# Kernel tuning notes

Hardware: AMD Instinct MI355X
Metric: run time of the kernel (lower is better)

Reference implementation:

```python
import jax, jax.numpy as jnp
import numpy as np

N_HEADS = 16
N_KV_HEADS = 4
HEAD_DIM = 128
ROPE_BASE = 10000.0


def _rms_norm(x):
    eps = jnp.asarray(jnp.finfo(x.dtype).eps, x.dtype)
    return x * jax.lax.rsqrt(jnp.mean(x * x, axis=-1, keepdims=True) + eps)


def _rope_tables(T, dtype):
    d = HEAD_DIM
    inv_freq = 1.0 / (ROPE_BASE ** (jnp.arange(0, d, 2, dtype=jnp.float32) / d))
    freqs = jnp.outer(jnp.arange(T, dtype=jnp.float32), inv_freq)  # [T, d/2]
    return jnp.cos(freqs).astype(dtype), jnp.sin(freqs).astype(dtype)


def _apply_rope(x, cos, sin):
    # x: [B, H, T, D]; cos/sin: [T, D/2]
    d = x.shape[-1] // 2
    x1, x2 = x[..., :d], x[..., d:]
    return jnp.concatenate((x1 * cos + x2 * sin, -x1 * sin + x2 * cos), axis=-1)


def setup_inputs() -> dict:
    key = jax.random.key(0)
    ks = jax.random.split(key, 5)
    B, T, C = 2, 2048, 2048
    kv_dim = N_KV_HEADS * HEAD_DIM
    s = 0.02
    return {
        "x": jax.random.normal(ks[0], (B, T, C), jnp.float32),
        "Wq": jax.random.normal(ks[1], (C, C), jnp.float32) * s,
        "Wk": jax.random.normal(ks[2], (kv_dim, C), jnp.float32) * s,
        "Wv": jax.random.normal(ks[3], (kv_dim, C), jnp.float32) * s,
        "Wo": jax.random.normal(ks[4], (C, C), jnp.float32) * s,
    }


def reference(x, Wq, Wk, Wv, Wo):
    B, T, C = x.shape
    g = N_HEADS // N_KV_HEADS

    # QKV projections (torch Linear: x @ W.T), split into heads -> [B, H, T, D]
    q = (x @ Wq.T).reshape(B, T, N_HEADS, HEAD_DIM).transpose(0, 2, 1, 3)
    k = (x @ Wk.T).reshape(B, T, N_KV_HEADS, HEAD_DIM).transpose(0, 2, 1, 3)
    v = (x @ Wv.T).reshape(B, T, N_KV_HEADS, HEAD_DIM).transpose(0, 2, 1, 3)

    # QK RMSNorm (no learned weight)
    q, k = _rms_norm(q), _rms_norm(k)

    # RoPE
    cos, sin = _rope_tables(T, q.dtype)
    q, k = _apply_rope(q, cos, sin), _apply_rope(k, cos, sin)

    # GQA: expand kv heads
    k = jnp.repeat(k, g, axis=1)
    v = jnp.repeat(v, g, axis=1)

    # causal SDPA
    scale = 1.0 / jnp.sqrt(jnp.asarray(HEAD_DIM, q.dtype))
    scores = jnp.einsum("bhqd,bhkd->bhqk", q, k) * scale
    mask = jnp.tril(jnp.ones((T, T), bool))
    scores = jnp.where(mask, scores, jnp.asarray(-jnp.inf, scores.dtype))
    att = jax.nn.softmax(scores, axis=-1)
    y = jnp.einsum("bhqk,bhkd->bhqd", att, v)

    y = y.transpose(0, 2, 1, 3).reshape(B, T, C)
    return y @ Wo.T
```

## Files before the change

### kernel.cpp

```cpp
#include <hip/hip_runtime.h>
#include <hip/hip_bf16.h>
#include <cstdint>
#include <math.h>

#define DEVINL __device__ __forceinline__

typedef __attribute__((ext_vector_type(8))) __bf16 bf16x8;
typedef __attribute__((ext_vector_type(4))) float floatx4;

constexpr int TB = 2;
constexpr int TT = 2048;
constexpr int TC = 2048;
constexpr int NH = 16, NKV = 4, HD = 128;
constexpr int MR = TB * TT;
constexpr int NQ = NH * HD;
constexpr int NK = NKV * HD;
constexpr int NQKV = NQ + 2 * NK;

DEVINL unsigned bfbits(float f) {
  unsigned u = __builtin_bit_cast(unsigned, f);
  return (u + 0x7FFFu + ((u >> 16) & 1u)) >> 16;
}
DEVINL int pack2bf(float lo, float hi) {
  return (int)(bfbits(lo) | (bfbits(hi) << 16));
}
DEVINL void gl_lds16(const __hip_bfloat16* g, __hip_bfloat16* l) {
  __builtin_amdgcn_global_load_lds(
      (const __attribute__((address_space(1))) unsigned int*)g,
      (__attribute__((address_space(3))) unsigned int*)l, 16, 0, 0);
}
DEVINL floatx4 mfma16(bf16x8 a, bf16x8 b, floatx4 c) {
  return __builtin_amdgcn_mfma_f32_16x16x32_bf16(a, b, c, 0, 0, 0);
}
DEVINL void cstore(float* p, float v) { *p = v; }
DEVINL void cstore(__hip_bfloat16* p, float v) { *(unsigned short*)p = (unsigned short)bfbits(v); }

__global__ __launch_bounds__(256) void k_cvt5(
    const float* __restrict__ s0, const float* __restrict__ s1,
    const float* __restrict__ s2, const float* __restrict__ s3,
    const float* __restrict__ s4,
    __hip_bfloat16* __restrict__ d0, __hip_bfloat16* __restrict__ d1,
    __hip_bfloat16* __restrict__ d2, __hip_bfloat16* __restrict__ d3,
    __hip_bfloat16* __restrict__ d4) {
  const float* s;
  __hip_bfloat16* d;
  int n;
  switch (blockIdx.y) {
    case 0: s = s0; d = d0; n = MR * TC; break;
    case 1: s = s1; d = d1; n = NQ * TC; break;
    case 2: s = s2; d = d2; n = NK * TC; break;
    case 3: s = s3; d = d3; n = NK * TC; break;
    default: s = s4; d = d4; n = TC * TC; break;
  }
  int i = (blockIdx.x * 256 + threadIdx.x) * 4;
  if (i >= n) return;
  float4 v = *(const float4*)(s + i);
  ushort4 o;
  o.x = (unsigned short)bfbits(v.x);
  o.y = (unsigned short)bfbits(v.y);
  o.z = (unsigned short)bfbits(v.z);
  o.w = (unsigned short)bfbits(v.w);
  *(ushort4*)(d + i) = o;
}

template <typename OUT_T>
__global__ __launch_bounds__(256, 2) void k_gemm_bt(
    const __hip_bfloat16* __restrict__ A, const __hip_bfloat16* __restrict__ B,
    OUT_T* __restrict__ C, int M, int N, int K) {
  __shared__ __align__(16) __hip_bfloat16 As[128 * 32];
  __shared__ __align__(16) __hip_bfloat16 Bs[128 * 32];
  const int tid = threadIdx.x;
  const int lane = tid & 63, w = tid >> 6;
  const int q15 = lane & 15, quad = lane >> 4;
  const int wm = w >> 1, wn = w & 1;
  const int tm = blockIdx.y, tn = blockIdx.x;

  const int r0 = tid >> 2, c0 = (tid & 3) * 8;
  const __hip_bfloat16* a0 = A + (size_t)(tm * 128 + r0) * K + c0;
  const __hip_bfloat16* a1 = A + (size_t)(tm * 128 + r0 + 64) * K + c0;
  const __hip_bfloat16* b0 = B + (size_t)(tn * 128 + r0) * K + c0;
  const __hip_bfloat16* b1 = B + (size_t)(tn * 128 + r0 + 64) * K + c0;
  __hip_bfloat16* lA0 = As + (tid & ~63) * 8;
  __hip_bfloat16* lA1 = As + 2048 + (tid & ~63) * 8;
  __hip_bfloat16* lB0 = Bs + (tid & ~63) * 8;
  __hip_bfloat16* lB1 = Bs + 2048 + (tid & ~63) * 8;

  floatx4 acc[4][4] = {};
  for (int k0 = 0; k0 < K; k0 += 32) {
    __syncthreads();
    gl_lds16(a0 + k0, lA0);
    gl_lds16(a1 + k0, lA1);
    gl_lds16(b0 + k0, lB0);
    gl_lds16(b1 + k0, lB1);
    __syncthreads();
    bf16x8 af[4], bfr[4];
#pragma unroll
    for (int i = 0; i < 4; i++)
      af[i] = *(const bf16x8*)(As + (wm * 64 + i * 16 + q15) * 32 + quad * 8);
#pragma unroll
    for (int i = 0; i < 4; i++)
      bfr[i] = *(const bf16x8*)(Bs + (wn * 64 + i * 16 + q15) * 32 + quad * 8);
#pragma unroll
    for (int mi = 0; mi < 4; mi++)
#pragma unroll
      for (int ni = 0; ni < 4; ni++)
        acc[mi][ni] = mfma16(af[mi], bfr[ni], acc[mi][ni]);
  }
#pragma unroll
  for (int mi = 0; mi < 4; mi++) {
    int row0 = tm * 128 + wm * 64 + mi * 16 + quad * 4;
#pragma unroll
    for (int ni = 0; ni < 4; ni++) {
      int col = tn * 128 + wn * 64 + ni * 16 + q15;
#pragma unroll
      for (int r = 0; r < 4; r++)
        cstore(C + (size_t)(row0 + r) * N + col, acc[mi][ni][r]);
    }
  }
}

__global__ __launch_bounds__(256) void k_ropenorm(
    const __hip_bfloat16* __restrict__ qkv,
    __hip_bfloat16* __restrict__ q_l, __hip_bfloat16* __restrict__ k_l) {
  int gw = (blockIdx.x * 256 + threadIdx.x) >> 6;
  int lane = threadIdx.x & 63;
  int head = gw % 20;
  int bt = gw / 20;
  int b = bt >> 11, t = bt & (TT - 1);
  bool isq = head < NH;
  int h = isq ? head : head - NH;
  const __hip_bfloat16* src = qkv + (size_t)bt * NQKV + (isq ? h * HD : NQ + h * HD);
  float x1 = __bfloat162float(src[lane]);
  float x2 = __bfloat162float(src[lane + 64]);
  float ss = x1 * x1 + x2 * x2;
#pragma unroll
  for (int m = 1; m < 64; m <<= 1) ss += __shfl_xor(ss, m, 64);
  float rinv = rsqrtf(ss * (1.0f / 128.0f) + 1.1920928955078125e-07f);
  float ang = (float)t * exp2f((float)lane * -(13.287712379549449f / 64.0f));
  float sv = sinf(ang), cv = cosf(ang);
  float scale = isq ? (1.4426950408889634f * 0.08838834764831845f) : 1.0f;
  float o1 = (x1 * cv + x2 * sv) * rinv * scale;
  float o2 = (x2 * cv - x1 * sv) * rinv * scale;
  __hip_bfloat16* dst = isq ? q_l + ((size_t)(b * NH + h) * TT + t) * HD
                            : k_l + ((size_t)(b * NKV + h) * TT + t) * HD;
  *(unsigned short*)(dst + lane) = (unsigned short)bfbits(o1);
  *(unsigned short*)(dst + lane + 64) = (unsigned short)bfbits(o2);
}

__global__ __launch_bounds__(256) void k_vtrans(const __hip_bfloat16* __restrict__ qkv,
                                                __hip_bfloat16* __restrict__ vt) {
  __shared__ __hip_bfloat16 tile[64][130];
  int bid = blockIdx.x;
  int t0 = (bid & 31) * 64;
  int hk = (bid >> 5) & 3;
  int b = bid >> 7;
  int tid = threadIdx.x;
#pragma unroll
  for (int j = 0; j < 32; j++) {
    int e = j * 256 + tid;
    int tt = e >> 7, d = e & 127;
    tile[tt][d] = qkv[(size_t)(b * TT + t0 + tt) * NQKV + NQ + NK + hk * HD + d];
  }
  __syncthreads();
#pragma unroll
  for (int j = 0; j < 32; j++) {
    int e = j * 256 + tid;
    int d = e >> 6, tt = e & 63;
    vt[(((size_t)(b * NKV + hk)) * HD + d) * TT + t0 + tt] = tile[tt][d];
  }
}

__global__ __launch_bounds__(256, 2) void k_attn(
    const __hip_bfloat16* __restrict__ q_l, const __hip_bfloat16* __restrict__ k_l,
    const __hip_bfloat16* __restrict__ vt_l, __hip_bfloat16* __restrict__ y) {
  __shared__ __align__(16) __hip_bfloat16 Ks[2][64 * 128];
  __shared__ __align__(16) __hip_bfloat16 Vs[2][128 * 64];
  const int tid = threadIdx.x, lane = tid & 63, w = tid >> 6;
  const int q15 = lane & 15, quad = lane >> 4;
  const int p = blockIdx.x;
  const int h = blockIdx.y, b = blockIdx.z;
  const int hk = h >> 2;

  const __hip_bfloat16* kbase = k_l + (size_t)(b * NKV + hk) * TT * HD;
  const __hip_bfloat16* vbase = vt_l + (size_t)(b * NKV + hk) * HD * TT;

  auto stage = [&](int kb, int buf) {
#pragma unroll
    for (int i = 0; i < 4; i++) {
      int s = i * 256 + tid;
      int rk = s >> 4, ck = s & 15;
      gl_lds16(kbase + (size_t)(kb * 64 + rk) * HD + (ck ^ (rk & 15)) * 8,
               Ks[buf] + (i * 256 + (tid & ~63)) * 8);
      int rv = s >> 3, cv = s & 7;
      gl_lds16(vbase + (size_t)rv * TT + kb * 64 + (cv ^ (rv & 7)) * 8,
               Vs[buf] + (i * 256 + (tid & ~63)) * 8);
    }
  };

  const int s0lane = ((quad & 1) << 1) * 16 + q15;
  const int s1lane = s0lane + 16;
  const bool hi = quad >= 2;
  int cur = 0;

  for (int ph = 0; ph < 2; ph++) {
    const int qb = ph ? (TT / 64 - 1 - p) : p;
    const __hip_bfloat16* qbase = q_l + ((size_t)(b * NH + h) * TT + qb * 64) * HD;

    bf16x8 qf[4];
#pragma unroll
    for (int dc = 0; dc < 4; dc++)
      qf[dc] = *(const bf16x8*)(qbase + (size_t)(w * 16 + q15) * HD + dc * 32 + quad * 8);

    floatx4 ot[8] = {};
    float m_run = -INFINITY, l_run = 0.0f;

    for (int kb = 0; kb <= qb; kb++) {
      __syncthreads();
      if (kb == 0) {
        stage(0, cur);
        __syncthreads();
      }
      if (kb < qb) stage(kb + 1, cur ^ 1);

      floatx4 st[4] = {};
#pragma unroll
      for (int kt = 0; kt < 4; kt++) {
        int r = kt * 16 + q15;
#pragma unroll
        for (int dc = 0; dc < 4; dc++) {
          int c = dc * 4 + quad;
          bf16x8 kf = *(const bf16x8*)(Ks[cur] + (r * 16 + (c ^ (r & 15))) * 8);
          st[kt] = mfma16(kf, qf[dc], st[kt]);
        }
      }
      if (kb == qb) {
        int qg = w * 16 + q15;
#pragma unroll
        for (int kt = 0; kt < 4; kt++)
#pragma unroll
          for (int r = 0; r < 4; r++)
            if (kt * 16 + quad * 4 + r > qg) st[kt][r] = -INFINITY;
      }
      float mloc = -INFINITY;
#pragma unroll
      for (int kt = 0; kt < 4; kt++)
#pragma unroll
        for (int r = 0; r < 4; r++) mloc = fmaxf(mloc, st[kt][r]);
      mloc = fmaxf(mloc, __shfl_xor(mloc, 16, 64));
      mloc = fmaxf(mloc, __shfl_xor(mloc, 32, 64));
      float m_new = fmaxf(m_run, mloc);
      float rsum = 0.f;
      int pk[4][2];
#pragma unroll
      for (int kt = 0; kt < 4; kt++) {
        float p0 = exp2f(st[kt][0] - m_new);
        float p1 = exp2f(st[kt][1] - m_new);
        float p2 = exp2f(st[kt][2] - m_new);
        float p3 = exp2f(st[kt][3] - m_new);
        rsum += (p0 + p1) + (p2 + p3);
        pk[kt][0] = pack2bf(p0, p1);
        pk[kt][1] = pack2bf(p2, p3);
      }
      rsum += __shfl_xor(rsum, 16, 64);
      rsum += __shfl_xor(rsum, 32, 64);
      if (__any(m_new > m_run)) {
        float alpha = exp2f(m_run - m_new);
        l_run *= alpha;
#pragma unroll
        for (int dt = 0; dt < 8; dt++) {
          ot[dt][0] *= alpha; ot[dt][1] *= alpha;
          ot[dt][2] *= alpha; ot[dt][3] *= alpha;
        }
      }
      l_run += rsum;
      m_run = m_new;

#pragma unroll
      for (int kc = 0; kc < 2; kc++) {
        int lo0 = __shfl(pk[kc * 2][0], s0lane, 64);
        int lo1 = __shfl(pk[kc * 2][1], s0lane, 64);
        int lo2 = __shfl(pk[kc * 2][0], s1lane, 64);
        int lo3 = __shfl(pk[kc * 2][1], s1lane, 64);
        int h0 = __shfl(pk[kc * 2 + 1][0], s0lane, 64);
        int h1 = __shfl(pk[kc * 2 + 1][1], s0lane, 64);
        int h2 = __shfl(pk[kc * 2 + 1][0], s1lane, 64);
        int h3 = __shfl(pk[kc * 2 + 1][1], s1lane, 64);
        union { int i[4]; bf16x8 v; } pu;
        pu.i[0] = hi ? h0 : lo0;
        pu.i[1] = hi ? h1 : lo1;
        pu.i[2] = hi ? h2 : lo2;
        pu.i[3] = hi ? h3 : lo3;
        bf16x8 pf = pu.v;
#pragma unroll
        for (int dt = 0; dt < 8; dt++) {
          int r = dt * 16 + q15, c = kc * 4 + quad;
          bf16x8 vf = *(const bf16x8*)(Vs[cur] + (r * 8 + (c ^ (r & 7))) * 8);
          ot[dt] = mfma16(vf, pf, ot[dt]);
        }
      }
      cur ^= 1;
    }
    float linv = 1.0f / l_run;
    int t = qb * 64 + w * 16 + q15;
    __hip_bfloat16* yrow = y + (size_t)(b * TT + t) * TC + h * HD;
#pragma unroll
    for (int dt = 0; dt < 8; dt++) {
      int d = dt * 16 + quad * 4;
      ushort4 o;
      o.x = (unsigned short)bfbits(ot[dt][0] * linv);
      o.y = (unsigned short)bfbits(ot[dt][1] * linv);
      o.z = (unsigned short)bfbits(ot[dt][2] * linv);
      o.w = (unsigned short)bfbits(ot[dt][3] * linv);
      *(ushort4*)(yrow + d) = o;
    }
  }
}

extern "C" void kernel_launch(void* const* d_in, const int* in_sizes, int n_in,
                              void* d_out, int out_size, void* d_ws, size_t ws_size,
                              hipStream_t stream) {
  (void)in_sizes; (void)n_in; (void)out_size; (void)ws_size;
  const float* x  = (const float*)d_in[0];
  const float* Wq = (const float*)d_in[1];
  const float* Wk = (const float*)d_in[2];
  const float* Wv = (const float*)d_in[3];
  const float* Wo = (const float*)d_in[4];
  float* out = (float*)d_out;

  char* ws = (char*)d_ws;
  size_t off = 0;
  auto alloc = [&](size_t bytes) {
    void* p = ws + off;
    off += (bytes + 255) & ~(size_t)255;
    return p;
  };
  __hip_bfloat16* xb   = (__hip_bfloat16*)alloc((size_t)MR * TC * 2);
  __hip_bfloat16* wqkv = (__hip_bfloat16*)alloc((size_t)NQKV * TC * 2);
  __hip_bfloat16* wo   = (__hip_bfloat16*)alloc((size_t)TC * TC * 2);
  __hip_bfloat16* qkv  = (__hip_bfloat16*)alloc((size_t)MR * NQKV * 2);
  __hip_bfloat16* q_l  = (__hip_bfloat16*)alloc((size_t)TB * NH * TT * HD * 2);
  __hip_bfloat16* k_l  = (__hip_bfloat16*)alloc((size_t)TB * NKV * TT * HD * 2);
  __hip_bfloat16* vt_l = (__hip_bfloat16*)alloc((size_t)TB * NKV * HD * TT * 2);
  __hip_bfloat16* yb   = (__hip_bfloat16*)alloc((size_t)MR * TC * 2);

  k_cvt5<<<dim3((MR * TC / 4 + 255) / 256, 5), 256, 0, stream>>>(
      x, Wq, Wk, Wv, Wo,
      xb, wqkv, wqkv + (size_t)NQ * TC, wqkv + (size_t)(NQ + NK) * TC, wo);

  k_gemm_bt<__hip_bfloat16><<<dim3(NQKV / 128, MR / 128), 256, 0, stream>>>(
      xb, wqkv, qkv, MR, NQKV, TC);

  k_ropenorm<<<(MR * 20) / 4, 256, 0, stream>>>(qkv, q_l, k_l);
  k_vtrans<<<TB * NKV * (TT / 64), 256, 0, stream>>>(qkv, vt_l);

  k_attn<<<dim3(TT / 64 / 2, NH, TB), 256, 0, stream>>>(q_l, k_l, vt_l, yb);

  k_gemm_bt<float><<<dim3(TC / 128, MR / 128), 256, 0, stream>>>(
      yb, wo, out, MR, TC, TC);
}
```

Baseline: 330.9 us.

## Drop online-softmax max tracking using bounded normalized scores; fuse prep kernels

Since Q and K are RMS-normalized, attention scores are bounded, so the kernel skips the running max, the per-block max reductions and the accumulator rescaling. It exponentiates directly and reduces the row sum only once at the end. The rope/norm and V-transpose kernels are merged into one launch to save launch overhead. Bf16 packing also switches to the library intrinsic. The trade-off is reliance on the score bound for numerical safety, and a small risk of precision loss in bf16 probabilities without max subtraction.

After: 320.6 us. -3.1%, faster.

```diff
diff --git a/kernel.cpp b/kernel.cpp
--- a/kernel.cpp
+++ b/kernel.cpp
@@ -21,8 +21,10 @@
   unsigned u = __builtin_bit_cast(unsigned, f);
   return (u + 0x7FFFu + ((u >> 16) & 1u)) >> 16;
 }
-DEVINL int pack2bf(float lo, float hi) {
-  return (int)(bfbits(lo) | (bfbits(hi) << 16));
+DEVINL int pk2(float a, float b) {
+  union { __hip_bfloat162 h; int i; } u;
+  u.h = __float22bfloat162_rn(float2{a, b});
+  return u.i;
 }
 DEVINL void gl_lds16(const __hip_bfloat16* g, __hip_bfloat16* l) {
   __builtin_amdgcn_global_load_lds(
@@ -119,54 +121,55 @@
   }
 }
 
-__global__ __launch_bounds__(256) void k_ropenorm(
+constexpr int ROPE_BLOCKS = (MR * 20) / 4;
+__global__ __launch_bounds__(256) void k_prep(
     const __hip_bfloat16* __restrict__ qkv,
-    __hip_bfloat16* __restrict__ q_l, __hip_bfloat16* __restrict__ k_l) {
-  int gw = (blockIdx.x * 256 + threadIdx.x) >> 6;
-  int lane = threadIdx.x & 63;
-  int head = gw % 20;
-  int bt = gw / 20;
-  int b = bt >> 11, t = bt & (TT - 1);
-  bool isq = head < NH;
-  int h = isq ? head : head - NH;
-  const __hip_bfloat16* src = qkv + (size_t)bt * NQKV + (isq ? h * HD : NQ + h * HD);
-  float x1 = __bfloat162float(src[lane]);
-  float x2 = __bfloat162float(src[lane + 64]);
-  float ss = x1 * x1 + x2 * x2;
-#pragma unroll
-  for (int m = 1; m < 64; m <<= 1) ss += __shfl_xor(ss, m, 64);
-  float rinv = rsqrtf(ss * (1.0f / 128.0f) + 1.1920928955078125e-07f);
-  float ang = (float)t * exp2f((float)lane * -(13.287712379549449f / 64.0f));
-  float sv = sinf(ang), cv = cosf(ang);
-  float scale = isq ? (1.4426950408889634f * 0.08838834764831845f) : 1.0f;
-  float o1 = (x1 * cv + x2 * sv) * rinv * scale;
-  float o2 = (x2 * cv - x1 * sv) * rinv * scale;
-  __hip_bfloat16* dst = isq ? q_l + ((size_t)(b * NH + h) * TT + t) * HD
-                            : k_l + ((size_t)(b * NKV + h) * TT + t) * HD;
-  *(unsigned short*)(dst + lane) = (unsigned short)bfbits(o1);
-  *(unsigned short*)(dst + lane + 64) = (unsigned short)bfbits(o2);
-}
-
-__global__ __launch_bounds__(256) void k_vtrans(const __hip_bfloat16* __restrict__ qkv,
-                                                __hip_bfloat16* __restrict__ vt) {
-  __shared__ __hip_bfloat16 tile[64][130];
-  int bid = blockIdx.x;
-  int t0 = (bid & 31) * 64;
-  int hk = (bid >> 5) & 3;
-  int b = bid >> 7;
-  int tid = threadIdx.x;
-#pragma unroll
-  for (int j = 0; j < 32; j++) {
-    int e = j * 256 + tid;
-    int tt = e >> 7, d = e & 127;
-    tile[tt][d] = qkv[(size_t)(b * TT + t0 + tt) * NQKV + NQ + NK + hk * HD + d];
-  }
-  __syncthreads();
-#pragma unroll
-  for (int j = 0; j < 32; j++) {
-    int e = j * 256 + tid;
-    int d = e >> 6, tt = e & 63;
-    vt[(((size_t)(b * NKV + hk)) * HD + d) * TT + t0 + tt] = tile[tt][d];
+    __hip_bfloat16* __restrict__ q_l, __hip_bfloat16* __restrict__ k_l,
+    __hip_bfloat16* __restrict__ vt) {
+  if (blockIdx.x < ROPE_BLOCKS) {
+    int gw = (blockIdx.x * 256 + threadIdx.x) >> 6;
+    int lane = threadIdx.x & 63;
+    int head = gw % 20;
+    int bt = gw / 20;
+    int b = bt >> 11, t = bt & (TT - 1);
+    bool isq = head < NH;
+    int h = isq ? head : head - NH;
+    const __hip_bfloat16* src = qkv + (size_t)bt * NQKV + (isq ? h * HD : NQ + h * HD);
+    float x1 = __bfloat162float(src[lane]);
+    float x2 = __bfloat162float(src[lane + 64]);
+    float ss = x1 * x1 + x2 * x2;
+#pragma unroll
+    for (int m = 1; m < 64; m <<= 1) ss += __shfl_xor(ss, m, 64);
+    float rinv = rsqrtf(ss * (1.0f / 128.0f) + 1.1920928955078125e-07f);
+    float ang = (float)t * exp2f((float)lane * -(13.287712379549449f / 64.0f));
+    float sv = sinf(ang), cv = cosf(ang);
+    float scale = isq ? (1.4426950408889634f * 0.08838834764831845f) : 1.0f;
+    float o1 = (x1 * cv + x2 * sv) * rinv * scale;
+    float o2 = (x2 * cv - x1 * sv) * rinv * scale;
+    __hip_bfloat16* dst = isq ? q_l + ((size_t)(b * NH + h) * TT + t) * HD
+                              : k_l + ((size_t)(b * NKV + h) * TT + t) * HD;
+    *(unsigned short*)(dst + lane) = (unsigned short)bfbits(o1);
+    *(unsigned short*)(dst + lane + 64) = (unsigned short)bfbits(o2);
+  } else {
+    __shared__ __hip_bfloat16 tile[64][130];
+    int bid = blockIdx.x - ROPE_BLOCKS;
+    int t0 = (bid & 31) * 64;
+    int hk = (bid >> 5) & 3;
+    int b = bid >> 7;
+    int tid = threadIdx.x;
+#pragma unroll
+    for (int j = 0; j < 32; j++) {
+      int e = j * 256 + tid;
+      int tt = e >> 7, d = e & 127;
+      tile[tt][d] = qkv[(size_t)(b * TT + t0 + tt) * NQKV + NQ + NK + hk * HD + d];
+    }
+    __syncthreads();
+#pragma unroll
+    for (int j = 0; j < 32; j++) {
+      int e = j * 256 + tid;
+      int d = e >> 6, tt = e & 63;
+      vt[(((size_t)(b * NKV + hk)) * HD + d) * TT + t0 + tt] = tile[tt][d];
+    }
   }
 }
 
@@ -212,7 +215,7 @@
       qf[dc] = *(const bf16x8*)(qbase + (size_t)(w * 16 + q15) * HD + dc * 32 + quad * 8);
 
     floatx4 ot[8] = {};
-    float m_run = -INFINITY, l_run = 0.0f;
+    float lsum = 0.0f;
 
     for (int kb = 0; kb <= qb; kb++) {
       __syncthreads();
@@ -241,40 +244,17 @@
           for (int r = 0; r < 4; r++)
             if (kt * 16 + quad * 4 + r > qg) st[kt][r] = -INFINITY;
       }
-      float mloc = -INFINITY;
-#pragma unroll
-      for (int kt = 0; kt < 4; kt++)
-#pragma unroll
-        for (int r = 0; r < 4; r++) mloc = fmaxf(mloc, st[kt][r]);
-      mloc = fmaxf(mloc, __shfl_xor(mloc, 16, 64));
-      mloc = fmaxf(mloc, __shfl_xor(mloc, 32, 64));
-      float m_new = fmaxf(m_run, mloc);
-      float rsum = 0.f;
       int pk[4][2];
 #pragma unroll
       for (int kt = 0; kt < 4; kt++) {
-        float p0 = exp2f(st[kt][0] - m_new);
-        float p1 = exp2f(st[kt][1] - m_new);
-        float p2 = exp2f(st[kt][2] - m_new);
-        float p3 = exp2f(st[kt][3] - m_new);
-        rsum += (p0 + p1) + (p2 + p3);
-        pk[kt][0] = pack2bf(p0, p1);
-        pk[kt][1] = pack2bf(p2, p3);
-      }
-      rsum += __shfl_xor(rsum, 16, 64);
-      rsum += __shfl_xor(rsum, 32, 64);
-      if (__any(m_new > m_run)) {
-        float alpha = exp2f(m_run - m_new);
-        l_run *= alpha;
-#pragma unroll
-        for (int dt = 0; dt < 8; dt++) {
-          ot[dt][0] *= alpha; ot[dt][1] *= alpha;
-          ot[dt][2] *= alpha; ot[dt][3] *= alpha;
-        }
-      }
-      l_run += rsum;
-      m_run = m_new;
-
+        float p0 = exp2f(st[kt][0]);
+        float p1 = exp2f(st[kt][1]);
+        float p2 = exp2f(st[kt][2]);
+        float p3 = exp2f(st[kt][3]);
+        lsum += (p0 + p1) + (p2 + p3);
+        pk[kt][0] = pk2(p0, p1);
+        pk[kt][1] = pk2(p2, p3);
+      }
 #pragma unroll
       for (int kc = 0; kc < 2; kc++) {
         int lo0 = __shfl(pk[kc * 2][0], s0lane, 64);
@@ -300,7 +280,9 @@
       }
       cur ^= 1;
     }
-    float linv = 1.0f / l_run;
+    lsum += __shfl_xor(lsum, 16, 64);
+    lsum += __shfl_xor(lsum, 32, 64);
+    float linv = 1.0f / lsum;
     int t = qb * 64 + w * 16 + q15;
     __hip_bfloat16* yrow = y + (size_t)(b * TT + t) * TC + h * HD;
 #pragma unroll
@@ -350,8 +332,7 @@
   k_gemm_bt<__hip_bfloat16><<<dim3(NQKV / 128, MR / 128), 256, 0, stream>>>(
       xb, wqkv, qkv, MR, NQKV, TC);
 
-  k_ropenorm<<<(MR * 20) / 4, 256, 0, stream>>>(qkv, q_l, k_l);
-  k_vtrans<<<TB * NKV * (TT / 64), 256, 0, stream>>>(qkv, vt_l);
+  k_prep<<<ROPE_BLOCKS + TB * NKV * (TT / 64), 256, 0, stream>>>(qkv, q_l, k_l, vt_l);
 
   k_attn<<<dim3(TT / 64 / 2, NH, TB), 256, 0, stream>>>(q_l, k_l, vt_l, yb);
 
```
